# Optimization experiments

Hardware: AMD Instinct MI355X
Metric: run time of the kernel (lower is better)

## Reference

```python
import jax, jax.numpy as jnp
import numpy as np

BN_EPS = 1e-5
DIST_EPS = 1e-8


def setup_inputs() -> dict:
    key = jax.random.key(0)
    ks = jax.random.split(key, 8)
    B, N, S = 8, 8192, 2048
    D_unk, D_kn = 128, 256
    inp = {
        "unknown_xyz": jax.random.uniform(ks[0], (B, N, 3), dtype=jnp.float32),
        "known_xyz": jax.random.uniform(ks[1], (B, S, 3), dtype=jnp.float32),
        "unknown_points": jax.random.normal(ks[2], (B, N, D_unk), dtype=jnp.float32),
        "known_points": jax.random.normal(ks[3], (B, S, D_kn), dtype=jnp.float32),
        "W0": jax.random.normal(ks[4], (256, 384), dtype=jnp.float32) * (1.0 / np.sqrt(384)),
        "b0": jnp.zeros((256,), jnp.float32),
        "g0": jnp.ones((256,), jnp.float32),
        "beta0": jnp.zeros((256,), jnp.float32),
        "W1": jax.random.normal(ks[5], (128, 256), dtype=jnp.float32) * (1.0 / np.sqrt(256)),
        "b1": jnp.zeros((128,), jnp.float32),
        "g1": jnp.ones((128,), jnp.float32),
        "beta1": jnp.zeros((128,), jnp.float32),
    }
    return inp


def _three_nn(unknown_xyz, known_xyz):
    # squared pairwise distances [B, N, S]
    d = jnp.sum((unknown_xyz[:, :, None, :] - known_xyz[:, None, :, :]) ** 2, axis=-1)
    neg_top, idx = jax.lax.top_k(-d, 3)  # 3 smallest distances
    return -neg_top, idx  # dists [B,N,3], idx [B,N,3]


def _conv_bn_relu(x, W, b, g, beta):
    # x: [B, N, Cin]; 1x1 Conv1d == per-point linear
    y = jnp.einsum("bnc,oc->bno", x, W) + b
    mean = jnp.mean(y, axis=(0, 1))
    var = jnp.var(y, axis=(0, 1))  # biased, as BatchNorm training forward
    y = g * (y - mean) * jax.lax.rsqrt(var + BN_EPS) + beta
    return jax.nn.relu(y)


def reference(unknown_xyz, known_xyz, unknown_points, known_points,
              W0, b0, g0, beta0, W1, b1, g1, beta1):
    dists, idx = _three_nn(unknown_xyz, known_xyz)
    dist_recip = 1.0 / (dists + DIST_EPS)
    weight = dist_recip / jnp.sum(dist_recip, axis=2, keepdims=True)  # [B,N,3]
    # gather 3 neighbor features: [B,N,3,D_kn]
    gathered = jax.vmap(lambda f, i: f[i])(known_points, idx)
    interpolated = jnp.sum(weight[..., None] * gathered, axis=2)  # [B,N,D_kn]
    x = jnp.concatenate([unknown_points, interpolated], axis=-1)  # [B,N,384]
    x = _conv_bn_relu(x, W0, b0, g0, beta0)
    x = _conv_bn_relu(x, W1, b1, g1, beta1)
    return x  # [B, N, 128]
```

## Files before the change

### kernel.cpp

```cpp
#include <hip/hip_runtime.h>
#include <hip/hip_bf16.h>


typedef __attribute__((ext_vector_type(8))) short short8;
typedef __attribute__((ext_vector_type(4))) float f32x4;

#define BB 8
#define NN 8192
#define SS 2048
#define M_TOT (BB * NN)
#define K1DIM 384
#define N1DIM 256
#define K2DIM 256
#define N2DIM 128
#define NCH 8
#define CHS (SS / NCH)
#define BK 64

#define KEY_MASK 0xFFFFF800u
#define IDX_MASK 0x7FFu

__device__ __forceinline__ unsigned short f2bf(float f) {
    unsigned int x = __float_as_uint(f);
    unsigned int r = x + 0x7fffu + ((x >> 16) & 1u);
    return (unsigned short)(r >> 16);
}
__device__ __forceinline__ float bf2f(unsigned short u) {
    return __uint_as_float(((unsigned int)u) << 16);
}
__device__ __forceinline__ unsigned int med3_u32(unsigned int a, unsigned int b,
                                                 unsigned int c) {
    unsigned int r;
    asm("v_med3_u32 %0, %1, %2, %3" : "=v"(r) : "v"(a), "v"(b), "v"(c));
    return r;
}

__device__ __forceinline__ void gload_lds16(const void* g, void* lds) {
    __builtin_amdgcn_global_load_lds(
        (const __attribute__((address_space(1))) unsigned int*)g,
        (__attribute__((address_space(3))) unsigned int*)lds, 16, 0, 0);
}

__global__ __launch_bounds__(256) void nn_cand_kernel(
    const float* __restrict__ uxyz,
    const float4* __restrict__ kpack,
    unsigned int* __restrict__ cand)
{
    const int tid  = threadIdx.x;
    const int bid  = blockIdx.x;
    const int ch   = bid & 7;
    const int tile = (bid >> 3) & 31;
    const int b    = bid >> 8;

    const int n = tile * 256 + tid;
    const float* up = uxyz + ((size_t)b * NN + n) * 3;
    const float ux = up[0], uy = up[1], uz = up[2];
    const float uu  = fmaf(ux, ux, fmaf(uy, uy, uz * uz));
    const float m2x = -2.0f * ux, m2y = -2.0f * uy, m2z = -2.0f * uz;

    const float4* kb = kpack + (size_t)b * SS + ch * CHS;
    const int base = ch * CHS;

    unsigned int k0 = 0xFFFFFFFFu, k1 = 0xFFFFFFFFu, k2 = 0xFFFFFFFFu;
#pragma unroll 8
    for (int s = 0; s < CHS; ++s) {
        float4 kc = kb[s];
        float d = kc.w + uu;
        d = fmaf(m2z, kc.z, d);
        d = fmaf(m2y, kc.y, d);
        d = fmaf(m2x, kc.x, d);
        d = fmaxf(d, 0.0f);
        unsigned int key = (__float_as_uint(d) & KEY_MASK) | (unsigned int)(base + s);
        unsigned int nk1 = med3_u32(k0, k1, key);
        unsigned int nk2 = med3_u32(k1, k2, key);
        k0 = min(k0, key);
        k1 = nk1;
        k2 = nk2;
    }

    const size_t pt = (size_t)b * NN + n;
    cand[(size_t)(ch * 3 + 0) * M_TOT + pt] = k0;
    cand[(size_t)(ch * 3 + 1) * M_TOT + pt] = k1;
    cand[(size_t)(ch * 3 + 2) * M_TOT + pt] = k2;
}

__global__ __launch_bounds__(256) void merge_interp_kernel(
    const unsigned int* __restrict__ cand,
    const float4* __restrict__ kpack,
    const float* __restrict__ uxyz,
    const float* __restrict__ upts,
    const float* __restrict__ kpts,
    unsigned short* __restrict__ x)
{
    __shared__ int   sidx[64][3];
    __shared__ float sw[64][3];

    const int tid = threadIdx.x;
    const int bid = blockIdx.x;
    const int b   = bid & 7;
    const int pn  = (bid >> 3) * 64;

    if (tid < 64) {
        const size_t pt = (size_t)b * NN + pn + tid;

        unsigned int k[6];
#pragma unroll
        for (int i = 0; i < 6; ++i) k[i] = 0xFFFFFFFFu;
#pragma unroll
        for (int ch = 0; ch < NCH; ++ch) {
#pragma unroll
            for (int j = 0; j < 3; ++j) {
                unsigned int t = cand[(size_t)(ch * 3 + j) * M_TOT + pt];
#pragma unroll
                for (int i = 0; i < 6; ++i) {
                    unsigned int a = min(k[i], t);
                    t = max(k[i], t);
                    k[i] = a;
                }
            }
        }

        const float* up = uxyz + pt * 3;
        const float ux = up[0], uy = up[1], uz = up[2];
        const float4* kpb4 = kpack + (size_t)b * SS;
        unsigned long long e[6];
#pragma unroll
        for (int i = 0; i < 6; ++i) {
            unsigned int idx = k[i] & IDX_MASK;
            float4 kc = kpb4[idx];
            float dx = kc.x - ux, dy = kc.y - uy, dz = kc.z - uz;
            float d = fmaf(dx, dx, fmaf(dy, dy, dz * dz));
            e[i] = ((unsigned long long)__float_as_uint(d) << 32) | idx;
        }
#pragma unroll
        for (int i = 0; i < 3; ++i)
#pragma unroll
            for (int j = i + 1; j < 6; ++j)
                if (e[j] < e[i]) { unsigned long long t = e[i]; e[i] = e[j]; e[j] = t; }

        float d0 = __uint_as_float((unsigned int)(e[0] >> 32));
        float d1 = __uint_as_float((unsigned int)(e[1] >> 32));
        float d2 = __uint_as_float((unsigned int)(e[2] >> 32));
        float r0 = 1.0f / (d0 + 1e-8f);
        float r1 = 1.0f / (d1 + 1e-8f);
        float r2 = 1.0f / (d2 + 1e-8f);
        float rs = 1.0f / (r0 + r1 + r2);
        sidx[tid][0] = (int)(e[0] & IDX_MASK);
        sidx[tid][1] = (int)(e[1] & IDX_MASK);
        sidx[tid][2] = (int)(e[2] & IDX_MASK);
        sw[tid][0] = r0 * rs; sw[tid][1] = r1 * rs; sw[tid][2] = r2 * rs;
    }
    __syncthreads();

    const int wv = tid >> 6, lane = tid & 63;
    const float* kpb = kpts + (size_t)b * SS * N1DIM;
    const float* upb = upts + (size_t)b * NN * 128;
    for (int p = wv; p < 64; p += 4) {
        const int j0 = sidx[p][0], j1 = sidx[p][1], j2 = sidx[p][2];
        const float w0 = sw[p][0], w1 = sw[p][1], w2 = sw[p][2];
        unsigned short* xr = x + ((size_t)b * NN + pn + p) * K1DIM;

        float4 f0 = *(const float4*)(kpb + (size_t)j0 * 256 + lane * 4);
        float4 f1 = *(const float4*)(kpb + (size_t)j1 * 256 + lane * 4);
        float4 f2 = *(const float4*)(kpb + (size_t)j2 * 256 + lane * 4);
        ushort4 o;
        o.x = f2bf(w0 * f0.x + w1 * f1.x + w2 * f2.x);
        o.y = f2bf(w0 * f0.y + w1 * f1.y + w2 * f2.y);
        o.z = f2bf(w0 * f0.z + w1 * f1.z + w2 * f2.z);
        o.w = f2bf(w0 * f0.w + w1 * f1.w + w2 * f2.w);
        *(ushort4*)(xr + 128 + lane * 4) = o;

        if (lane < 32) {
            float4 u = *(const float4*)(upb + ((size_t)(pn + p)) * 128 + lane * 4);
            ushort4 q;
            q.x = f2bf(u.x); q.y = f2bf(u.y); q.z = f2bf(u.z); q.w = f2bf(u.w);
            *(ushort4*)(xr + lane * 4) = q;
        }
    }
}

__global__ __launch_bounds__(256) void cvt_w_kernel(
    const float* __restrict__ W0, const float* __restrict__ W1,
    const float* __restrict__ kxyz,
    unsigned short* __restrict__ Wb0, unsigned short* __restrict__ Wb1,
    float4* __restrict__ kpack)
{
    int i = blockIdx.x * 256 + threadIdx.x;
    if (i < N1DIM * K1DIM) Wb0[i] = f2bf(W0[i]);
    if (i < N2DIM * K2DIM) Wb1[i] = f2bf(W1[i]);
    if (i < BB * SS) {
        const float* p = kxyz + (size_t)i * 3;
        float px = p[0], py = p[1], pz = p[2];
        kpack[i] = make_float4(px, py, pz, fmaf(px, px, fmaf(py, py, pz * pz)));
    }
}

#define G1_NT (K1DIM / BK)
__global__ __launch_bounds__(512, 2) void gemm1_kernel(
    const unsigned short* __restrict__ X,
    const unsigned short* __restrict__ Wb,
    unsigned short* __restrict__ Y,
    float* __restrict__ stats)
{
    __shared__ __align__(128) unsigned char smem[2 * 49152];

    const int tid = threadIdx.x;
    const int l = tid & 63, w = tid >> 6;
    const int wm = w >> 2, wn = w & 3;
    const int row0 = blockIdx.x * 128;
    const int srow = l >> 3;
    const int sbo  = (l & 7) * 16;

    f32x4 acc[4][4];
#pragma unroll
    for (int m = 0; m < 4; ++m)
#pragma unroll
        for (int n = 0; n < 4; ++n) {
            f32x4 z = {0.f, 0.f, 0.f, 0.f};
            acc[m][n] = z;
        }

    const unsigned char* Xb = (const unsigned char*)X;
    const unsigned char* Bb = (const unsigned char*)Wb;

    auto stage = [&](int buf, int t) {
        unsigned char* Al = smem + buf * 49152;
        unsigned char* Bl = Al + 16384;
        const int k0b = t * (BK * 2);
#pragma unroll
        for (int i = 0; i < 2; ++i) {
            const int r = w * 16 + i * 8 + srow;
            gload_lds16(Xb + (size_t)(row0 + r) * (K1DIM * 2) + k0b + (sbo ^ ((r & 7) << 4)),
                        Al + r * 128 + sbo);
        }
#pragma unroll
        for (int i = 0; i < 4; ++i) {
            const int r = w * 32 + i * 8 + srow;
            gload_lds16(Bb + (size_t)r * (K1DIM * 2) + k0b + (sbo ^ ((r & 7) << 4)),
                        Bl + r * 128 + sbo);
        }
    };

    auto compute = [&](int buf) {
        const unsigned char* Al = smem + buf * 49152;
        const unsigned char* Bl = Al + 16384;
#pragma unroll
        for (int ks = 0; ks < 2; ++ks) {
            const int bo = ks * 64 + (l >> 4) * 16;
            short8 a[4], bq[4];
#pragma unroll
            for (int m = 0; m < 4; ++m) {
                const int r = wm * 64 + m * 16 + (l & 15);
                a[m] = *(const short8*)(Al + r * 128 + (bo ^ ((r & 7) << 4)));
            }
#pragma unroll
            for (int n = 0; n < 4; ++n) {
                const int r = wn * 64 + n * 16 + (l & 15);
                bq[n] = *(const short8*)(Bl + r * 128 + (bo ^ ((r & 7) << 4)));
            }
#pragma unroll
            for (int m = 0; m < 4; ++m)
#pragma unroll
                for (int n = 0; n < 4; ++n)
                    acc[m][n] = __builtin_amdgcn_mfma_f32_16x16x32_bf16(
                        a[m], bq[n], acc[m][n], 0, 0, 0);
        }
    };

    stage(0, 0);
    __syncthreads();
#pragma unroll
    for (int t = 0; t < G1_NT; ++t) {
        const int cur = t & 1;
        if (t + 1 < G1_NT) stage(cur ^ 1, t + 1);
        compute(cur);
        __syncthreads();
    }

    float s1[4] = {0.f, 0.f, 0.f, 0.f}, s2[4] = {0.f, 0.f, 0.f, 0.f};
#pragma unroll
    for (int m = 0; m < 4; ++m) {
        const int row = row0 + wm * 64 + m * 16 + (l >> 4) * 4;
#pragma unroll
        for (int n = 0; n < 4; ++n) {
            const int col = wn * 64 + n * 16 + (l & 15);
            f32x4 v = acc[m][n];
#pragma unroll
            for (int r = 0; r < 4; ++r) {
                float f = v[r];
                Y[(size_t)(row + r) * N1DIM + col] = f2bf(f);
                s1[n] += f;
                s2[n] += f * f;
            }
        }
    }
#pragma unroll
    for (int n = 0; n < 4; ++n) {
        s1[n] += __shfl_xor(s1[n], 16, 64);
        s1[n] += __shfl_xor(s1[n], 32, 64);
        s2[n] += __shfl_xor(s2[n], 16, 64);
        s2[n] += __shfl_xor(s2[n], 32, 64);
    }
    if (l < 16) {
#pragma unroll
        for (int n = 0; n < 4; ++n) {
            const int col = wn * 64 + n * 16 + l;
            atomicAdd(&stats[col], s1[n]);
            atomicAdd(&stats[N1DIM + col], s2[n]);
        }
    }
}

#define G2_NT (K2DIM / BK)
__global__ __launch_bounds__(512, 4) void gemm2_kernel(
    const unsigned short* __restrict__ Y0,
    const unsigned short* __restrict__ Wb,
    const float* __restrict__ stats0,
    const float* __restrict__ g0,
    const float* __restrict__ beta0,
    float* __restrict__ Y1,
    float* __restrict__ stats)
{
    __shared__ __align__(128) unsigned char smem[2 * 32768];
    __shared__ float sgm[K2DIM], sga[K2DIM];

    const int tid = threadIdx.x;
    const int l = tid & 63, w = tid >> 6;
    const int wm = w >> 2, wn = w & 3;
    const int row0 = blockIdx.x * 128;
    const int srow = l >> 3;
    const int sbo  = (l & 7) * 16;
    const int lr  = tid >> 2;
    const int lcq = tid & 3;

    f32x4 acc[4][2];
#pragma unroll
    for (int m = 0; m < 4; ++m)
#pragma unroll
        for (int n = 0; n < 2; ++n) {
            f32x4 z = {0.f, 0.f, 0.f, 0.f};
            acc[m][n] = z;
        }

    const unsigned char* Bb = (const unsigned char*)Wb;
    short8 areg0, areg1;

    auto issueA = [&](int t) {
        const unsigned short* src = Y0 + (size_t)(row0 + lr) * K2DIM + t * BK + lcq * 16;
        areg0 = *(const short8*)src;
        areg1 = *(const short8*)(src + 8);
    };
    auto stageB = [&](int buf, int t) {
        unsigned char* Bl = smem + buf * 32768 + 16384;
        const int k0b = t * (BK * 2);
#pragma unroll
        for (int i = 0; i < 2; ++i) {
            const int r = w * 16 + i * 8 + srow;
            gload_lds16(Bb + (size_t)r * (K2DIM * 2) + k0b + (sbo ^ ((r & 7) << 4)),
                        Bl + r * 128 + sbo);
        }
    };
    auto xformA = [&](int buf, int t) {
        unsigned char* Al = smem + buf * 32768;
        const int kb = t * BK + lcq * 16;
        short8 o0, o1;
#pragma unroll
        for (int j = 0; j < 8; ++j) {
            float f = bf2f((unsigned short)areg0[j]);
            f = fmaxf(fmaf(f, sgm[kb + j], sga[kb + j]), 0.f);
            o0[j] = (short)f2bf(f);
            float g = bf2f((unsigned short)areg1[j]);
            g = fmaxf(fmaf(g, sgm[kb + 8 + j], sga[kb + 8 + j]), 0.f);
            o1[j] = (short)f2bf(g);
        }
        const int bo = lcq * 32;
        *(short8*)(Al + lr * 128 + ((bo) ^ ((lr & 7) << 4))) = o0;
        *(short8*)(Al + lr * 128 + ((bo + 16) ^ ((lr & 7) << 4))) = o1;
    };
    auto compute = [&](int buf) {
        const unsigned char* Al = smem + buf * 32768;
        const unsigned char* Bl = Al + 16384;
#pragma unroll
        for (int ks = 0; ks < 2; ++ks) {
            const int bo = ks * 64 + (l >> 4) * 16;
            short8 a[4], bq[2];
#pragma unroll
            for (int m = 0; m < 4; ++m) {
                const int r = wm * 64 + m * 16 + (l & 15);
                a[m] = *(const short8*)(Al + r * 128 + (bo ^ ((r & 7) << 4)));
            }
#pragma unroll
            for (int n = 0; n < 2; ++n) {
                const int r = wn * 32 + n * 16 + (l & 15);
                bq[n] = *(const short8*)(Bl + r * 128 + (bo ^ ((r & 7) << 4)));
            }
#pragma unroll
            for (int m = 0; m < 4; ++m)
#pragma unroll
                for (int n = 0; n < 2; ++n)
                    acc[m][n] = __builtin_amdgcn_mfma_f32_16x16x32_bf16(
                        a[m], bq[n], acc[m][n], 0, 0, 0);
        }
    };

    if (tid < K2DIM) {
        const float inv = 1.0f / (float)M_TOT;
        float mean = stats0[tid] * inv;
        float var  = stats0[N1DIM + tid] * inv - mean * mean;
        float m = g0[tid] * rsqrtf(var + 1e-5f);
        sgm[tid] = m;
        sga[tid] = beta0[tid] - mean * m;
    }
    issueA(0);
    stageB(0, 0);
    __syncthreads();
    xformA(0, 0);
    __syncthreads();

#pragma unroll
    for (int t = 0; t < G2_NT; ++t) {
        const int cur = t & 1;
        if (t + 1 < G2_NT) { issueA(t + 1); stageB(cur ^ 1, t + 1); }
        compute(cur);
        if (t + 1 < G2_NT) xformA(cur ^ 1, t + 1);
        __syncthreads();
    }

    float s1[2] = {0.f, 0.f}, s2[2] = {0.f, 0.f};
#pragma unroll
    for (int m = 0; m < 4; ++m) {
        const int row = row0 + wm * 64 + m * 16 + (l >> 4) * 4;
#pragma unroll
        for (int n = 0; n < 2; ++n) {
            const int col = wn * 32 + n * 16 + (l & 15);
            f32x4 v = acc[m][n];
#pragma unroll
            for (int r = 0; r < 4; ++r) {
                float f = v[r];
                Y1[(size_t)(row + r) * N2DIM + col] = f;
                s1[n] += f;
                s2[n] += f * f;
            }
        }
    }
#pragma unroll
    for (int n = 0; n < 2; ++n) {
        s1[n] += __shfl_xor(s1[n], 16, 64);
        s1[n] += __shfl_xor(s1[n], 32, 64);
        s2[n] += __shfl_xor(s2[n], 16, 64);
        s2[n] += __shfl_xor(s2[n], 32, 64);
    }
    if (l < 16) {
#pragma unroll
        for (int n = 0; n < 2; ++n) {
            const int col = wn * 32 + n * 16 + l;
            atomicAdd(&stats[col], s1[n]);
            atomicAdd(&stats[N2DIM + col], s2[n]);
        }
    }
}

__global__ __launch_bounds__(256) void bn_out_kernel(
    const float* __restrict__ Y1, const float* __restrict__ stats1,
    const float* __restrict__ g1, const float* __restrict__ beta1,
    float* __restrict__ out)
{
    __shared__ float sgm[N2DIM], sga[N2DIM];
    const int tid = threadIdx.x;
    if (tid < N2DIM) {
        const float inv = 1.0f / (float)M_TOT;
        float mean = stats1[tid] * inv;
        float var  = stats1[N2DIM + tid] * inv - mean * mean;
        float m = g1[tid] * rsqrtf(var + 1e-5f);
        sgm[tid] = m;
        sga[tid] = beta1[tid] - mean * m;
    }
    __syncthreads();

    const int total = M_TOT * N2DIM / 4;
    for (int i = blockIdx.x * 256 + tid; i < total; i += gridDim.x * 256) {
        float4 v = ((const float4*)Y1)[i];
        const int cg = (i & 31) * 4;
        float4 m = *(const float4*)(sgm + cg);
        float4 a = *(const float4*)(sga + cg);
        float4 o;
        o.x = fmaxf(fmaf(v.x, m.x, a.x), 0.f);
        o.y = fmaxf(fmaf(v.y, m.y, a.y), 0.f);
        o.z = fmaxf(fmaf(v.z, m.z, a.z), 0.f);
        o.w = fmaxf(fmaf(v.w, m.w, a.w), 0.f);
        ((float4*)out)[i] = o;
    }
}

extern "C" void kernel_launch(void* const* d_in, const int* in_sizes, int n_in,
                              void* d_out, int out_size, void* d_ws, size_t ws_size,
                              hipStream_t stream)
{
    const float* uxyz  = (const float*)d_in[0];
    const float* kxyz  = (const float*)d_in[1];
    const float* upts  = (const float*)d_in[2];
    const float* kpts  = (const float*)d_in[3];
    const float* W0    = (const float*)d_in[4];
    const float* g0    = (const float*)d_in[6];
    const float* beta0 = (const float*)d_in[7];
    const float* W1    = (const float*)d_in[8];
    const float* g1    = (const float*)d_in[10];
    const float* beta1 = (const float*)d_in[11];
    float* out = (float*)d_out;

    char* ws = (char*)d_ws;
    const size_t off_x   = 0;
    const size_t off_y0  = 50331648;
    const size_t off_w0  = off_y0 + 33554432;
    const size_t off_w1  = off_w0 + 196608;
    const size_t off_f   = off_w1 + 65536;

    unsigned short* x    = (unsigned short*)(ws + off_x);
    float*          y1   = (float*)(ws + off_x);
    unsigned short* y0   = (unsigned short*)(ws + off_y0);
    unsigned int*   cand = (unsigned int*)(ws + off_y0);
    float4*         kpack = (float4*)(ws + off_y0 + 8388608);
    unsigned short* wb0  = (unsigned short*)(ws + off_w0);
    unsigned short* wb1  = (unsigned short*)(ws + off_w1);
    float* F = (float*)(ws + off_f);
    float* stats0 = F;
    float* stats1 = F + 512;

    hipMemsetAsync(stats0, 0, 768 * sizeof(float), stream);

    cvt_w_kernel<<<384, 256, 0, stream>>>(W0, W1, kxyz, wb0, wb1, kpack);
    nn_cand_kernel<<<2048, 256, 0, stream>>>(uxyz, kpack, cand);
    merge_interp_kernel<<<1024, 256, 0, stream>>>(cand, kpack, uxyz, upts, kpts, x);
    gemm1_kernel<<<M_TOT / 128, 512, 0, stream>>>(x, wb0, y0, stats0);
    gemm2_kernel<<<M_TOT / 128, 512, 0, stream>>>(y0, wb1, stats0, g0, beta0, y1, stats1);
    bn_out_kernel<<<2048, 256, 0, stream>>>(y1, stats1, g1, beta1, out);
}
```

Baseline: 155.9 us.

## Project known features through W0 before interpolation, then gather projected rows

Result: slower. 218.4 us (+40.1%).

```diff
diff --git a/kernel.cpp b/kernel.cpp
--- a/kernel.cpp
+++ b/kernel.cpp
@@ -9,7 +9,6 @@
 #define NN 8192
 #define SS 2048
 #define M_TOT (BB * NN)
-#define K1DIM 384
 #define N1DIM 256
 #define K2DIM 256
 #define N2DIM 128
@@ -84,109 +83,77 @@
     cand[(size_t)(ch * 3 + 2) * M_TOT + pt] = k2;
 }
 
-__global__ __launch_bounds__(256) void merge_interp_kernel(
+__global__ __launch_bounds__(256) void merge_w_kernel(
     const unsigned int* __restrict__ cand,
     const float4* __restrict__ kpack,
     const float* __restrict__ uxyz,
-    const float* __restrict__ upts,
-    const float* __restrict__ kpts,
-    unsigned short* __restrict__ x)
-{
-    __shared__ int   sidx[64][3];
-    __shared__ float sw[64][3];
-
-    const int tid = threadIdx.x;
-    const int bid = blockIdx.x;
-    const int b   = bid & 7;
-    const int pn  = (bid >> 3) * 64;
-
-    if (tid < 64) {
-        const size_t pt = (size_t)b * NN + pn + tid;
-
-        unsigned int k[6];
-#pragma unroll
-        for (int i = 0; i < 6; ++i) k[i] = 0xFFFFFFFFu;
-#pragma unroll
-        for (int ch = 0; ch < NCH; ++ch) {
-#pragma unroll
-            for (int j = 0; j < 3; ++j) {
-                unsigned int t = cand[(size_t)(ch * 3 + j) * M_TOT + pt];
-#pragma unroll
-                for (int i = 0; i < 6; ++i) {
-                    unsigned int a = min(k[i], t);
-                    t = max(k[i], t);
-                    k[i] = a;
-                }
+    uint4* __restrict__ widx)
+{
+    const size_t pt = (size_t)blockIdx.x * 256 + threadIdx.x;
+    const int b = (int)(pt >> 13);
+
+    unsigned int k[6];
+#pragma unroll
+    for (int i = 0; i < 6; ++i) k[i] = 0xFFFFFFFFu;
+#pragma unroll
+    for (int ch = 0; ch < NCH; ++ch) {
+#pragma unroll
+        for (int j = 0; j < 3; ++j) {
+            unsigned int t = cand[(size_t)(ch * 3 + j) * M_TOT + pt];
+#pragma unroll
+            for (int i = 0; i < 6; ++i) {
+                unsigned int a = min(k[i], t);
+                t = max(k[i], t);
+                k[i] = a;
             }
         }
-
-        const float* up = uxyz + pt * 3;
-        const float ux = up[0], uy = up[1], uz = up[2];
-        const float4* kpb4 = kpack + (size_t)b * SS;
-        unsigned long long e[6];
-#pragma unroll
-        for (int i = 0; i < 6; ++i) {
-            unsigned int idx = k[i] & IDX_MASK;
-            float4 kc = kpb4[idx];
-            float dx = kc.x - ux, dy = kc.y - uy, dz = kc.z - uz;
-            float d = fmaf(dx, dx, fmaf(dy, dy, dz * dz));
-            e[i] = ((unsigned long long)__float_as_uint(d) << 32) | idx;
-        }
-#pragma unroll
-        for (int i = 0; i < 3; ++i)
-#pragma unroll
-            for (int j = i + 1; j < 6; ++j)
-                if (e[j] < e[i]) { unsigned long long t = e[i]; e[i] = e[j]; e[j] = t; }
-
-        float d0 = __uint_as_float((unsigned int)(e[0] >> 32));
-        float d1 = __uint_as_float((unsigned int)(e[1] >> 32));
-        float d2 = __uint_as_float((unsigned int)(e[2] >> 32));
-        float r0 = 1.0f / (d0 + 1e-8f);
-        float r1 = 1.0f / (d1 + 1e-8f);
-        float r2 = 1.0f / (d2 + 1e-8f);
-        float rs = 1.0f / (r0 + r1 + r2);
-        sidx[tid][0] = (int)(e[0] & IDX_MASK);
-        sidx[tid][1] = (int)(e[1] & IDX_MASK);
-        sidx[tid][2] = (int)(e[2] & IDX_MASK);
-        sw[tid][0] = r0 * rs; sw[tid][1] = r1 * rs; sw[tid][2] = r2 * rs;
-    }
-    __syncthreads();
-
-    const int wv = tid >> 6, lane = tid & 63;
-    const float* kpb = kpts + (size_t)b * SS * N1DIM;
-    const float* upb = upts + (size_t)b * NN * 128;
-    for (int p = wv; p < 64; p += 4) {
-        const int j0 = sidx[p][0], j1 = sidx[p][1], j2 = sidx[p][2];
-        const float w0 = sw[p][0], w1 = sw[p][1], w2 = sw[p][2];
-        unsigned short* xr = x + ((size_t)b * NN + pn + p) * K1DIM;
-
-        float4 f0 = *(const float4*)(kpb + (size_t)j0 * 256 + lane * 4);
-        float4 f1 = *(const float4*)(kpb + (size_t)j1 * 256 + lane * 4);
-        float4 f2 = *(const float4*)(kpb + (size_t)j2 * 256 + lane * 4);
-        ushort4 o;
-        o.x = f2bf(w0 * f0.x + w1 * f1.x + w2 * f2.x);
-        o.y = f2bf(w0 * f0.y + w1 * f1.y + w2 * f2.y);
-        o.z = f2bf(w0 * f0.z + w1 * f1.z + w2 * f2.z);
-        o.w = f2bf(w0 * f0.w + w1 * f1.w + w2 * f2.w);
-        *(ushort4*)(xr + 128 + lane * 4) = o;
-
-        if (lane < 32) {
-            float4 u = *(const float4*)(upb + ((size_t)(pn + p)) * 128 + lane * 4);
-            ushort4 q;
-            q.x = f2bf(u.x); q.y = f2bf(u.y); q.z = f2bf(u.z); q.w = f2bf(u.w);
-            *(ushort4*)(xr + lane * 4) = q;
-        }
-    }
+    }
+
+    const float* up = uxyz + pt * 3;
+    const float ux = up[0], uy = up[1], uz = up[2];
+    const float4* kpb4 = kpack + (size_t)b * SS;
+    unsigned long long e[6];
+#pragma unroll
+    for (int i = 0; i < 6; ++i) {
+        unsigned int idx = k[i] & IDX_MASK;
+        float4 kc = kpb4[idx];
+        float dx = kc.x - ux, dy = kc.y - uy, dz = kc.z - uz;
+        float d = fmaf(dx, dx, fmaf(dy, dy, dz * dz));
+        e[i] = ((unsigned long long)__float_as_uint(d) << 32) | idx;
+    }
+#pragma unroll
+    for (int i = 0; i < 3; ++i)
+#pragma unroll
+        for (int j = i + 1; j < 6; ++j)
+            if (e[j] < e[i]) { unsigned long long t = e[i]; e[i] = e[j]; e[j] = t; }
+
+    float d0 = __uint_as_float((unsigned int)(e[0] >> 32));
+    float d1 = __uint_as_float((unsigned int)(e[1] >> 32));
+    float d2 = __uint_as_float((unsigned int)(e[2] >> 32));
+    float r0 = 1.0f / (d0 + 1e-8f);
+    float r1 = 1.0f / (d1 + 1e-8f);
+    float r2 = 1.0f / (d2 + 1e-8f);
+    float rs = 1.0f / (r0 + r1 + r2);
+    unsigned int i0 = (unsigned int)(e[0] & IDX_MASK);
+    unsigned int i1 = (unsigned int)(e[1] & IDX_MASK);
+    unsigned int i2 = (unsigned int)(e[2] & IDX_MASK);
+    widx[pt] = make_uint4(__float_as_uint(r0 * rs), __float_as_uint(r1 * rs),
+                          i0 | (i1 << 16), i2);
 }
 
 __global__ __launch_bounds__(256) void cvt_w_kernel(
     const float* __restrict__ W0, const float* __restrict__ W1,
     const float* __restrict__ kxyz,
-    unsigned short* __restrict__ Wb0, unsigned short* __restrict__ Wb1,
-    float4* __restrict__ kpack)
+    unsigned short* __restrict__ Wa, unsigned short* __restrict__ Wb,
+    unsigned short* __restrict__ Wb1, float4* __restrict__ kpack)
 {
     int i = blockIdx.x * 256 + threadIdx.x;
-    if (i < N1DIM * K1DIM) Wb0[i] = f2bf(W0[i]);
+    if (i < 256 * 384) {
+        int o = i / 384, c = i - o * 384;
+        unsigned short v = f2bf(W0[i]);
+        if (c < 128) Wa[o * 128 + c] = v;
+        else         Wb[o * 256 + (c - 128)] = v;
+    }
     if (i < N2DIM * K2DIM) Wb1[i] = f2bf(W1[i]);
     if (i < BB * SS) {
         const float* p = kxyz + (size_t)i * 3;
@@ -195,21 +162,162 @@
     }
 }
 
-#define G1_NT (K1DIM / BK)
-__global__ __launch_bounds__(512, 2) void gemm1_kernel(
-    const unsigned short* __restrict__ X,
+__global__ __launch_bounds__(512, 4) void zgemm_kernel(
+    const float* __restrict__ kpts,
     const unsigned short* __restrict__ Wb,
-    unsigned short* __restrict__ Y,
+    unsigned short* __restrict__ Z)
+{
+    __shared__ __align__(128) unsigned char smem[2 * 32768];
+
+    const int tid = threadIdx.x;
+    const int l = tid & 63, w = tid >> 6;
+    const int wm = w >> 2, wn = w & 3;
+    const int mt = blockIdx.x >> 1, nh = blockIdx.x & 1;
+    const int row0 = mt * 128;
+    const int srow = l >> 3, sbo = (l & 7) * 16;
+    const int lr = tid >> 2, lcq = tid & 3;
+
+    f32x4 acc[4][2];
+#pragma unroll
+    for (int m = 0; m < 4; ++m)
+#pragma unroll
+        for (int n = 0; n < 2; ++n) {
+            f32x4 z = {0.f, 0.f, 0.f, 0.f};
+            acc[m][n] = z;
+        }
+
+    const unsigned char* Bb = (const unsigned char*)Wb + (size_t)nh * 128 * 512;
+    float4 af0, af1, af2, af3;
+
+    auto issueA = [&](int t) {
+        const float* src = kpts + (size_t)(row0 + lr) * 256 + t * 64 + lcq * 16;
+        af0 = ((const float4*)src)[0];
+        af1 = ((const float4*)src)[1];
+        af2 = ((const float4*)src)[2];
+        af3 = ((const float4*)src)[3];
+    };
+    auto stageB = [&](int buf, int t) {
+        unsigned char* Bl = smem + buf * 32768 + 16384;
+#pragma unroll
+        for (int i = 0; i < 2; ++i) {
+            const int r = w * 16 + i * 8 + srow;
+            gload_lds16(Bb + (size_t)r * 512 + t * 128 + (sbo ^ ((r & 7) << 4)),
+                        Bl + r * 128 + sbo);
+        }
+    };
+    auto xformA = [&](int buf) {
+        unsigned char* Al = smem + buf * 32768;
+        short8 o0, o1;
+        o0[0] = (short)f2bf(af0.x); o0[1] = (short)f2bf(af0.y);
+        o0[2] = (short)f2bf(af0.z); o0[3] = (short)f2bf(af0.w);
+        o0[4] = (short)f2bf(af1.x); o0[5] = (short)f2bf(af1.y);
+        o0[6] = (short)f2bf(af1.z); o0[7] = (short)f2bf(af1.w);
+        o1[0] = (short)f2bf(af2.x); o1[1] = (short)f2bf(af2.y);
+        o1[2] = (short)f2bf(af2.z); o1[3] = (short)f2bf(af2.w);
+        o1[4] = (short)f2bf(af3.x); o1[5] = (short)f2bf(af3.y);
+        o1[6] = (short)f2bf(af3.z); o1[7] = (short)f2bf(af3.w);
+        const int bo = lcq * 32;
+        *(short8*)(Al + lr * 128 + ((bo) ^ ((lr & 7) << 4))) = o0;
+        *(short8*)(Al + lr * 128 + ((bo + 16) ^ ((lr & 7) << 4))) = o1;
+    };
+    auto compute = [&](int buf) {
+        const unsigned char* Al = smem + buf * 32768;
+        const unsigned char* Bl = Al + 16384;
+#pragma unroll
+        for (int ks = 0; ks < 2; ++ks) {
+            const int bo = ks * 64 + (l >> 4) * 16;
+            short8 a[4], bq[2];
+#pragma unroll
+            for (int m = 0; m < 4; ++m) {
+                const int r = wm * 64 + m * 16 + (l & 15);
+                a[m] = *(const short8*)(Al + r * 128 + (bo ^ ((r & 7) << 4)));
+            }
+#pragma unroll
+            for (int n = 0; n < 2; ++n) {
+                const int r = wn * 32 + n * 16 + (l & 15);
+                bq[n] = *(const short8*)(Bl + r * 128 + (bo ^ ((r & 7) << 4)));
+            }
+#pragma unroll
+            for (int m = 0; m < 4; ++m)
+#pragma unroll
+                for (int n = 0; n < 2; ++n)
+                    acc[m][n] = __builtin_amdgcn_mfma_f32_16x16x32_bf16(
+                        a[m], bq[n], acc[m][n], 0, 0, 0);
+        }
+    };
+
+    issueA(0);
+    stageB(0, 0);
+    xformA(0);
+    __syncthreads();
+#pragma unroll
+    for (int t = 0; t < 4; ++t) {
+        const int cur = t & 1;
+        if (t + 1 < 4) { issueA(t + 1); stageB(cur ^ 1, t + 1); }
+        compute(cur);
+        if (t + 1 < 4) xformA(cur ^ 1);
+        __syncthreads();
+    }
+
+#pragma unroll
+    for (int m = 0; m < 4; ++m) {
+        const int row = row0 + wm * 64 + m * 16 + (l >> 4) * 4;
+#pragma unroll
+        for (int n = 0; n < 2; ++n) {
+            const int col = nh * 128 + wn * 32 + n * 16 + (l & 15);
+            f32x4 v = acc[m][n];
+#pragma unroll
+            for (int r = 0; r < 4; ++r)
+                Z[(size_t)(row + r) * 256 + col] = f2bf(v[r]);
+        }
+    }
+}
+
+__global__ __launch_bounds__(512, 2) void gemm1c_kernel(
+    const float* __restrict__ upts,
+    const unsigned short* __restrict__ Wa,
+    const unsigned short* __restrict__ Z,
+    const uint4* __restrict__ widx,
+    unsigned short* __restrict__ Y0,
     float* __restrict__ stats)
 {
-    __shared__ __align__(128) unsigned char smem[2 * 49152];
+    __shared__ __align__(128) unsigned char smem[98304];
 
     const int tid = threadIdx.x;
     const int l = tid & 63, w = tid >> 6;
     const int wm = w >> 2, wn = w & 3;
     const int row0 = blockIdx.x * 128;
-    const int srow = l >> 3;
-    const int sbo  = (l & 7) * 16;
+    const int lr = tid >> 2, lcq = tid & 3;
+
+    {
+        const unsigned char* Bb = (const unsigned char*)Wa;
+#pragma unroll
+        for (int i = 0; i < 8; ++i) {
+            const int off = w * 8192 + i * 1024 + l * 16;
+            const int r = off >> 8;
+            const int inner = (l & 15) * 16;
+            gload_lds16(Bb + r * 256 + (inner ^ ((r & 7) << 4)),
+                        smem + 32768 + off);
+        }
+    }
+    {
+        const float* src = upts + (size_t)(row0 + lr) * 128 + lcq * 32;
+        float4 f[8];
+#pragma unroll
+        for (int q = 0; q < 8; ++q) f[q] = ((const float4*)src)[q];
+#pragma unroll
+        for (int q = 0; q < 4; ++q) {
+            float4 fa = f[q * 2], fb = f[q * 2 + 1];
+            short8 o;
+            o[0] = (short)f2bf(fa.x); o[1] = (short)f2bf(fa.y);
+            o[2] = (short)f2bf(fa.z); o[3] = (short)f2bf(fa.w);
+            o[4] = (short)f2bf(fb.x); o[5] = (short)f2bf(fb.y);
+            o[6] = (short)f2bf(fb.z); o[7] = (short)f2bf(fb.w);
+            *(short8*)(smem + lr * 256 +
+                       ((lcq * 64 + q * 16) ^ ((lr & 7) << 4))) = o;
+        }
+    }
+    __syncthreads();
 
     f32x4 acc[4][4];
 #pragma unroll
@@ -219,81 +327,83 @@
             f32x4 z = {0.f, 0.f, 0.f, 0.f};
             acc[m][n] = z;
         }
-
-    const unsigned char* Xb = (const unsigned char*)X;
-    const unsigned char* Bb = (const unsigned char*)Wb;
-
-    auto stage = [&](int buf, int t) {
-        unsigned char* Al = smem + buf * 49152;
-        unsigned char* Bl = Al + 16384;
-        const int k0b = t * (BK * 2);
-#pragma unroll
-        for (int i = 0; i < 2; ++i) {
-            const int r = w * 16 + i * 8 + srow;
-            gload_lds16(Xb + (size_t)(row0 + r) * (K1DIM * 2) + k0b + (sbo ^ ((r & 7) << 4)),
-                        Al + r * 128 + sbo);
-        }
-#pragma unroll
-        for (int i = 0; i < 4; ++i) {
-            const int r = w * 32 + i * 8 + srow;
-            gload_lds16(Bb + (size_t)r * (K1DIM * 2) + k0b + (sbo ^ ((r & 7) << 4)),
-                        Bl + r * 128 + sbo);
-        }
-    };
-
-    auto compute = [&](int buf) {
-        const unsigned char* Al = smem + buf * 49152;
-        const unsigned char* Bl = Al + 16384;
-#pragma unroll
-        for (int ks = 0; ks < 2; ++ks) {
-            const int bo = ks * 64 + (l >> 4) * 16;
-            short8 a[4], bq[4];
+#pragma unroll
+    for (int ks = 0; ks < 4; ++ks) {
+        const int bo = ks * 64 + (l >> 4) * 16;
+        short8 a[4], bq[4];
+#pragma unroll
+        for (int m = 0; m < 4; ++m) {
+            const int r = wm * 64 + m * 16 + (l & 15);
+            a[m] = *(const short8*)(smem + r * 256 + (bo ^ ((r & 7) << 4)));
+        }
+#pragma unroll
+        for (int n = 0; n < 4; ++n) {
+            const int r = wn * 64 + n * 16 + (l & 15);
+            bq[n] = *(const short8*)(smem + 32768 + r * 256 + (bo ^ ((r & 7) << 4)));
+        }
+#pragma unroll
+        for (int m = 0; m < 4; ++m)
+#pragma unroll
+            for (int n = 0; n < 4; ++n)
+                acc[m][n] = __builtin_amdgcn_mfma_f32_16x16x32_bf16(
+                    a[m], bq[n], acc[m][n], 0, 0, 0);
+    }
+    __syncthreads();
+
+    const int bb = row0 >> 13;
+    const unsigned char* Zb = (const unsigned char*)Z + (size_t)bb * 2048 * 512;
+    float s1[4] = {0.f, 0.f, 0.f, 0.f}, s2[4] = {0.f, 0.f, 0.f, 0.f};
+
+    for (int c = 0; c < 2; ++c) {
+        if (c) __syncthreads();
+#pragma unroll
+        for (int i = 0; i < 12; ++i) {
+            const int rr = w * 24 + i * 2 + (l >> 5);
+            const int p = rr / 3;
+            const int j = rr - p * 3;
+            const size_t pt = (size_t)row0 + c * 64 + p;
+            uint4 wv = widx[pt];
+            unsigned int idx = (j == 2) ? wv.w
+                             : ((j == 1) ? (wv.z >> 16) : (wv.z & 0xFFFFu));
+            gload_lds16(Zb + (size_t)idx * 512 + (((l & 31) * 16) ^ ((rr & 7) << 4)),
+                        smem + (w * 24 + i * 2) * 512 + l * 16);
+        }
+        __syncthreads();
+        if (wm == c) {
 #pragma unroll
             for (int m = 0; m < 4; ++m) {
-                const int r = wm * 64 + m * 16 + (l & 15);
-                a[m] = *(const short8*)(Al + r * 128 + (bo ^ ((r & 7) << 4)));
+#pragma unroll
+                for (int r = 0; r < 4; ++r) {
+                    const int p_loc = m * 16 + ((l >> 4) << 2) + r;
+                    const size_t pt = (size_t)row0 + c * 64 + p_loc;
+                    uint4 wv = widx[pt];
+                    const float w0 = __uint_as_float(wv.x);
+                    const float w1 = __uint_as_float(wv.y);
+                    const float w2 = 1.0f - w0 - w1;
+                    const int rb = p_loc * 3 * 512;
+#pragma unroll
+                    for (int n = 0; n < 4; ++n) {
+                        const int col = wn * 64 + n * 16 + (l & 15);
+                        const int cb = col * 2;
+                        float z0 = bf2f(*(const unsigned short*)(
+                            smem + rb + (cb ^ (((p_loc * 3) & 7) << 4))));
+                        float z1 = bf2f(*(const unsigned short*)(
+                            smem + rb + 512 + (cb ^ (((p_loc * 3 + 1) & 7) << 4))));
+                        float z2 = bf2f(*(const unsigned short*)(
+                            smem + rb + 1024 + (cb ^ (((p_loc * 3 + 2) & 7) << 4))));
+                        float f = acc[m][n][r];
+                        f = fmaf(w0, z0, f);
+                        f = fmaf(w1, z1, f);
+                        f = fmaf(w2, z2, f);
+                        Y0[pt * 256 + col] = f2bf(f);
+                        s1[n] += f;
+                        s2[n] += f * f;
+                    }
+                }
             }
-#pragma unroll
-            for (int n = 0; n < 4; ++n) {
-                const int r = wn * 64 + n * 16 + (l & 15);
-                bq[n] = *(const short8*)(Bl + r * 128 + (bo ^ ((r & 7) << 4)));
-            }
-#pragma unroll
-            for (int m = 0; m < 4; ++m)
-#pragma unroll
-                for (int n = 0; n < 4; ++n)
-                    acc[m][n] = __builtin_amdgcn_mfma_f32_16x16x32_bf16(
-                        a[m], bq[n], acc[m][n], 0, 0, 0);
-        }
-    };
-
-    stage(0, 0);
-    __syncthreads();
-#pragma unroll
-    for (int t = 0; t < G1_NT; ++t) {
-        const int cur = t & 1;
-        if (t + 1 < G1_NT) stage(cur ^ 1, t + 1);
-        compute(cur);
-        __syncthreads();
-    }
-
-    float s1[4] = {0.f, 0.f, 0.f, 0.f}, s2[4] = {0.f, 0.f, 0.f, 0.f};
-#pragma unroll
-    for (int m = 0; m < 4; ++m) {
-        const int row = row0 + wm * 64 + m * 16 + (l >> 4) * 4;
-#pragma unroll
-        for (int n = 0; n < 4; ++n) {
-            const int col = wn * 64 + n * 16 + (l & 15);
-            f32x4 v = acc[m][n];
-#pragma unroll
-            for (int r = 0; r < 4; ++r) {
-                float f = v[r];
-                Y[(size_t)(row + r) * N1DIM + col] = f2bf(f);
-                s1[n] += f;
-                s2[n] += f * f;
-            }
-        }
-    }
+        }
+    }
+
 #pragma unroll
     for (int n = 0; n < 4; ++n) {
         s1[n] += __shfl_xor(s1[n], 16, 64);
@@ -509,18 +619,23 @@
     float* out = (float*)d_out;
 
     char* ws = (char*)d_ws;
-    const size_t off_x   = 0;
-    const size_t off_y0  = 50331648;
-    const size_t off_w0  = off_y0 + 33554432;
-    const size_t off_w1  = off_w0 + 196608;
-    const size_t off_f   = off_w1 + 65536;
-
-    unsigned short* x    = (unsigned short*)(ws + off_x);
-    float*          y1   = (float*)(ws + off_x);
+    const size_t off_y1 = 0;
+    const size_t off_wx = 35651584;
+    const size_t off_z  = 36700160;
+    const size_t off_y0 = 50331648;
+    const size_t off_wa = 83886080;
+    const size_t off_wb = 83951616;
+    const size_t off_w1 = 84082688;
+    const size_t off_f  = 84148224;
+
+    float*          y1   = (float*)(ws + off_y1);
+    uint4*          widx = (uint4*)(ws + off_wx);
+    unsigned short* Zb   = (unsigned short*)(ws + off_z);
     unsigned short* y0   = (unsigned short*)(ws + off_y0);
     unsigned int*   cand = (unsigned int*)(ws + off_y0);
     float4*         kpack = (float4*)(ws + off_y0 + 8388608);
-    unsigned short* wb0  = (unsigned short*)(ws + off_w0);
+    unsigned short* wa   = (unsigned short*)(ws + off_wa);
+    unsigned short* wb   = (unsigned short*)(ws + off_wb);
     unsigned short* wb1  = (unsigned short*)(ws + off_w1);
     float* F = (float*)(ws + off_f);
     float* stats0 = F;
@@ -528,10 +643,11 @@
 
     hipMemsetAsync(stats0, 0, 768 * sizeof(float), stream);
 
-    cvt_w_kernel<<<384, 256, 0, stream>>>(W0, W1, kxyz, wb0, wb1, kpack);
+    cvt_w_kernel<<<384, 256, 0, stream>>>(W0, W1, kxyz, wa, wb, wb1, kpack);
     nn_cand_kernel<<<2048, 256, 0, stream>>>(uxyz, kpack, cand);
-    merge_interp_kernel<<<1024, 256, 0, stream>>>(cand, kpack, uxyz, upts, kpts, x);
-    gemm1_kernel<<<M_TOT / 128, 512, 0, stream>>>(x, wb0, y0, stats0);
-    gemm2_kernel<<<M_TOT / 128, 512, 0, stream>>>(y0, wb1, stats0, g0, beta0, y1, stats1);
+    merge_w_kernel<<<256, 256, 0, stream>>>(cand, kpack, uxyz, widx);
+    zgemm_kernel<<<256, 512, 0, stream>>>(kpts, wb, Zb);
+    gemm1c_kernel<<<512, 512, 0, stream>>>(upts, wa, Zb, widx, y0, stats0);
+    gemm2_kernel<<<512, 512, 0, stream>>>(y0, wb1, stats0, g0, beta0, y1, stats1);
     bn_out_kernel<<<2048, 256, 0, stream>>>(y1, stats1, g1, beta1, out);
 }
```
